# Kernel tuning notes

Hardware: AMD Instinct MI355X
Metric: run time of the kernel (lower is better)

Reference implementation:

```python
import jax, jax.numpy as jnp
import numpy as np

A = 8        # n_agents
NACT = 16    # n_actions
R = 64       # rnn_hidden_dim
OBS = 128    # obs_shape
ATTN = 64    # attn_dim
HID = 256    # hidden_dim
INP = 152    # input_shape = obs + n_actions + n_agents
E = 2048     # episode_num
TW = 1.0     # teammate_loss_weight
WW = 1.0     # world_loss_weight


def _lin(key, out_d, in_d):
    k1, k2 = jax.random.split(key)
    s = 1.0 / np.sqrt(in_d)
    w = jax.random.uniform(k1, (out_d, in_d), minval=-s, maxval=s, dtype=jnp.float32)
    b = jax.random.uniform(k2, (out_d,), minval=-s, maxval=s, dtype=jnp.float32)
    return w, b


def setup_inputs() -> dict:
    key = jax.random.key(0)
    ks = jax.random.split(key, 16)
    rows = E * A
    d = {}
    d['inputs'] = jax.random.normal(ks[0], (rows, INP), dtype=jnp.float32)
    d['hidden_state'] = jax.random.normal(ks[1], (rows, R), dtype=jnp.float32)
    d['obs'] = jax.random.normal(ks[2], (rows, OBS), dtype=jnp.float32)
    d['obs_next'] = jax.random.normal(ks[3], (rows, OBS), dtype=jnp.float32)
    d['u'] = jax.random.randint(ks[4], (rows, 1), 0, NACT, dtype=jnp.int64 if jax.config.jax_enable_x64 else jnp.int32)
    d['fc1_w'], d['fc1_b'] = _lin(ks[5], R, INP)
    d['gru_w_ih'], d['gru_b_ih'] = _lin(ks[6], 3 * R, R)
    d['gru_w_hh'], d['gru_b_hh'] = _lin(ks[7], 3 * R, R)
    d['tm_w1'], d['tm_b1'] = _lin(ks[8], HID, R + A)
    d['tm_w2'], d['tm_b2'] = _lin(ks[9], NACT, HID)
    d['wm_w1'], d['wm_b1'] = _lin(ks[10], HID, OBS + A * NACT)
    d['wm_w2'], d['wm_b2'] = _lin(ks[11], OBS, HID)
    d['wq_w'], d['wq_b'] = _lin(ks[12], ATTN, 2 * OBS)
    d['wk_w'], d['wk_b'] = _lin(ks[13], ATTN, NACT)
    d['wv1_w'], d['wv1_b'] = _lin(ks[14], ATTN, R + NACT)
    d['wv2_w'], d['wv2_b'] = _lin(ks[15], NACT, ATTN)
    return d


def reference(inputs, hidden_state, obs, obs_next, u,
              fc1_w, fc1_b, gru_w_ih, gru_b_ih, gru_w_hh, gru_b_hh,
              tm_w1, tm_b1, tm_w2, tm_b2,
              wm_w1, wm_b1, wm_w2, wm_b2,
              wq_w, wq_b, wk_w, wk_b, wv1_w, wv1_b, wv2_w, wv2_b):
    sg = jax.lax.stop_gradient
    rows = inputs.shape[0]
    Ep = rows // A  # episode_num

    # --- GRU agent trunk ---
    x = jax.nn.relu(inputs @ fc1_w.T + fc1_b)
    h_in = hidden_state.reshape(-1, R)
    gi = x @ gru_w_ih.T + gru_b_ih
    gh = h_in @ gru_w_hh.T + gru_b_hh
    i_r, i_z, i_n = jnp.split(gi, 3, axis=-1)
    h_r, h_z, h_n = jnp.split(gh, 3, axis=-1)
    r = jax.nn.sigmoid(i_r + h_r)
    z = jax.nn.sigmoid(i_z + h_z)
    n = jnp.tanh(i_n + r * h_n)
    h = (1.0 - z) * n + z * h_in  # (rows, R)

    eyeA = jnp.eye(A, dtype=h.dtype)
    off = 1.0 - eyeA  # (A,A) zero on diagonal

    # --- teammate model: h_repeat[e,i,j] = h[e,j] with diagonal zeroed ---
    hd = sg(h).reshape(Ep, A, R)
    hr = jnp.broadcast_to(hd[:, None, :, :], (Ep, A, A, R)) * off[None, :, :, None]
    dj = jnp.broadcast_to(eyeA[None, None], (Ep, A, A, A)) * off[None, :, :, None]
    inp_t = jnp.concatenate([hr.reshape(-1, R), dj.reshape(-1, A)], axis=-1)
    actions = jax.nn.relu(inp_t @ tm_w1.T + tm_b1) @ tm_w2.T + tm_b2  # (Ep*A*A, NACT)

    # --- teammate CE loss (masked mean over all Ep*A*A rows) ---
    labels = jnp.broadcast_to(u.reshape(Ep, 1, A), (Ep, A, A)).reshape(-1)
    mask = jnp.broadcast_to(off[None], (Ep, A, A)).reshape(-1)
    logp = jax.nn.log_softmax(actions, axis=-1)
    ce = -jnp.take_along_axis(logp, labels[:, None], axis=1)[:, 0]
    loss1 = (ce * mask).mean() * TW

    # --- mask own action, world model ---
    am = (actions.reshape(Ep, A, A, NACT) * off[None, :, :, None]).reshape(rows, A, NACT)
    am_det = sg(am)
    w_in = jnp.concatenate([obs, am_det.reshape(rows, A * NACT)], axis=-1)
    o_next_hat = jax.nn.relu(w_in @ wm_w1.T + wm_b1) @ wm_w2.T + wm_b2  # (rows, OBS)
    loss2 = jnp.mean((o_next_hat - obs_next) ** 2) * WW

    # --- reflection: masked attention aggregation over teammates ---
    query = jnp.concatenate([obs, sg(o_next_hat)], axis=-1) @ wq_w.T + wq_b  # (rows, ATTN)
    key = (am_det.reshape(-1, NACT) @ wk_w.T + wk_b).reshape(rows, A, ATTN)
    hrep = jnp.broadcast_to(h.reshape(Ep, 1, A, R), (Ep, A, A, R)).reshape(-1, R)
    inps_v = jnp.concatenate([hrep, am_det.reshape(-1, NACT)], axis=-1)
    value = (jax.nn.relu(inps_v @ wv1_w.T + wv1_b) @ wv2_w.T + wv2_b).reshape(rows, A, NACT)
    scores = jnp.einsum('bd,bjd->bj', query / jnp.sqrt(jnp.float32(ATTN)), key).reshape(Ep, A, A)
    scores = jnp.where(eyeA[None].astype(bool), jnp.float32(-1e9), scores)  # self-exclusion
    attn = jax.nn.softmax(scores, axis=-1).reshape(rows, A, 1)
    q_reflect = jnp.sum(value * attn, axis=1)  # (rows, NACT)

    return q_reflect, h, loss1, loss2
```

## Files before the change

kernel.cpp:

```cpp
#include <hip/hip_runtime.h>
#include <math.h>

#define E_NUM 2048
#define A_N   8
#define ROWS  (E_NUM*A_N)
#define TRUNK_BLOCKS 512
#define TRUNK_EXTRA  108

typedef __attribute__((ext_vector_type(8))) short bf16x8;
typedef __attribute__((ext_vector_type(4))) float f32x4;

__device__ __forceinline__ unsigned short f2bf(float x) {
  unsigned int u = __float_as_uint(x);
  return (unsigned short)((u + 0x7FFFu + ((u >> 16) & 1u)) >> 16);
}
__device__ __forceinline__ ushort4 f2bf4(float4 v) {
  return make_ushort4(f2bf(v.x), f2bf(v.y), f2bf(v.z), f2bf(v.w));
}
__device__ __forceinline__ float bf2f(unsigned short u) {
  return __uint_as_float(((unsigned int)u) << 16);
}
#define MFMA16(a,b,c) __builtin_amdgcn_mfma_f32_16x16x32_bf16(a,b,c,0,0,0)

#define T_WK   0
#define T_WV1  1024
#define T_WV2  6144
#define TMB    7168
#define B_WM1  9216
#define B_WM2  41984
#define B_WQ   58368
#define B_TM1  66560
#define B_TM2  74752
#define B_FC1  76800
#define B_WIH  81920
#define B_WHH  88064
#define O_ACT  94208
#define O_QRY  356352
#define O_L1P  1404928
#define O_L2P  1405440

#define DO_H   262144
#define DO_L1  1310720
#define DO_L2  1310721

#define LD4(p) (*(const float4*)(p))

struct PrepP {
  const float* tsrc[3]; int tO[3], tK[3], tOff[3];
  const float* ssrc[8]; int sO[8], sK[8], sKs[8], sSt[8], sOff[8];
  const float* tm_w1; const float* tm_b1;
};

__global__ __launch_bounds__(256) void k_prep(PrepP p, float* __restrict__ ws,
                                              unsigned short* __restrict__ wsu) {
  int bid = blockIdx.x;
  int m = 5 + (bid >> 4), sub = bid & 15;
  const float* src = p.ssrc[m];
  unsigned short* dst = wsu + p.sOff[m];
  int K = p.sK[m], Ks = p.sKs[m], stride = p.sSt[m], n = p.sO[m] * K, S = K >> 5;
  for (int f = sub * 256 + threadIdx.x; f < n; f += 16 * 256) {
    int j = f & 7, l = (f >> 3) & 63, rest = f >> 9;
    int s = rest % S, c = rest / S;
    int row = c * 16 + (l & 15), col = s * 32 + ((l >> 4) << 3) + j;
    dst[f] = (col < Ks) ? f2bf(src[row * stride + col]) : (unsigned short)0;
  }
}

__global__ __launch_bounds__(512, 4) void k_trunk(
    const float* __restrict__ inp, const float* __restrict__ hin,
    const unsigned short* __restrict__ fc1bf, const unsigned short* __restrict__ wihbf,
    const unsigned short* __restrict__ whhbf,
    const float* __restrict__ fc1_b, const float* __restrict__ bih, const float* __restrict__ bhh,
    float* __restrict__ hout, PrepP p, float* __restrict__ ws_f,
    unsigned short* __restrict__ wsu)
{
  __shared__ __align__(16) unsigned short in_b[32 * 168];
  __shared__ __align__(16) unsigned short x_b[32 * 72];
  __shared__ __align__(16) unsigned short h_b[32 * 72];
  int tid = threadIdx.x, w = tid >> 6, lane = tid & 63;
  int lo = lane & 15, hi = lane >> 4;

  if (blockIdx.x >= TRUNK_BLOCKS) {
    int eb = blockIdx.x - TRUNK_BLOCKS;
    if (eb < 24) {
      int b = eb >> 3, sl = eb & 7;
      const float* s = p.tsrc[b];
      float* d = ws_f + p.tOff[b];
      int O = p.tO[b], K = p.tK[b], n = O * K;
      for (int i = sl * 512 + tid; i < n; i += 8 * 512) {
        int o = i / K, k = i - o * K;
        d[k * O + o] = s[i];
      }
    } else if (eb < 104) {
      int q = eb - 24, m = q >> 4, sub = q & 15;
      const float* src = p.ssrc[m];
      unsigned short* dst = wsu + p.sOff[m];
      int K = p.sK[m], Ks = p.sKs[m], stride = p.sSt[m], n = p.sO[m] * K, S = K >> 5;
      for (int f = sub * 512 + tid; f < n; f += 16 * 512) {
        int j = f & 7, l = (f >> 3) & 63, rest = f >> 9;
        int s = rest % S, c = rest / S;
        int row = c * 16 + (l & 15), col = s * 32 + ((l >> 4) << 3) + j;
        dst[f] = (col < Ks) ? f2bf(src[row * stride + col]) : (unsigned short)0;
      }
    } else {
      int i = (eb - 104) * 512 + tid;
      int j = i >> 8, o = i & 255;
      ws_f[TMB + i] = p.tm_b1[o] + p.tm_w1[o * 72 + 64 + j];
    }
    return;
  }

  int row0 = blockIdx.x * 32;
  int c = w & 3, rt = w >> 2;

  for (int i = tid; i < 1216; i += 512) {
    int e = i << 2;
    int r = e / 152, cc = e - r * 152;
    float4 v = LD4(inp + (size_t)(row0 + r) * 152 + cc);
    *(ushort4*)(in_b + r * 168 + cc) = f2bf4(v);
  }
  if (tid < 256) { int r = tid >> 3, cc = tid & 7; in_b[r * 168 + 152 + cc] = 0; }
  {
    int r = tid >> 4, cc = (tid & 15) << 2;
    float4 v = LD4(hin + (size_t)(row0 + r) * 64 + cc);
    *(ushort4*)(h_b + r * 72 + cc) = f2bf4(v);
  }
  __syncthreads();

  bf16x8 wf1[5];
#pragma unroll
  for (int s = 0; s < 5; s++)
    wf1[s] = *(const bf16x8*)(fc1bf + (size_t)((c * 5 + s) * 64 + lane) * 8);
  f32x4 acc = {0, 0, 0, 0};
#pragma unroll
  for (int s = 0; s < 5; s++) {
    bf16x8 af = *(const bf16x8*)(in_b + (rt * 16 + lo) * 168 + s * 32 + hi * 8);
    acc = MFMA16(af, wf1[s], acc);
  }
  float fb = fc1_b[16 * c + lo];
#pragma unroll
  for (int r = 0; r < 4; r++)
    x_b[(rt * 16 + hi * 4 + r) * 72 + 16 * c + lo] = f2bf(fmaxf(acc[r] + fb, 0.f));
  __syncthreads();

  bf16x8 wfi[3][2], wfh[3][2];
#pragma unroll
  for (int t = 0; t < 3; t++)
#pragma unroll
    for (int s = 0; s < 2; s++) {
      int chunk = c + 4 * t;
      wfi[t][s] = *(const bf16x8*)(wihbf + (size_t)((chunk * 2 + s) * 64 + lane) * 8);
      wfh[t][s] = *(const bf16x8*)(whhbf + (size_t)((chunk * 2 + s) * 64 + lane) * 8);
    }
  f32x4 ai[3], ah[3];
#pragma unroll
  for (int t = 0; t < 3; t++) { ai[t] = {0,0,0,0}; ah[t] = {0,0,0,0}; }
#pragma unroll
  for (int s = 0; s < 2; s++) {
    bf16x8 ax  = *(const bf16x8*)(x_b + (rt * 16 + lo) * 72 + s * 32 + hi * 8);
    bf16x8 ahv = *(const bf16x8*)(h_b + (rt * 16 + lo) * 72 + s * 32 + hi * 8);
#pragma unroll
    for (int t = 0; t < 3; t++) {
      ai[t] = MFMA16(ax,  wfi[t][s], ai[t]);
      ah[t] = MFMA16(ahv, wfh[t][s], ah[t]);
    }
  }
  int col = 16 * c + lo;
  float b_ir = bih[col],       b_hr = bhh[col];
  float b_iz = bih[64 + col],  b_hz = bhh[64 + col];
  float b_in = bih[128 + col], b_hn = bhh[128 + col];
#pragma unroll
  for (int r = 0; r < 4; r++) {
    size_t grow = (size_t)(row0 + rt * 16 + hi * 4 + r);
    float rg = 1.f / (1.f + expf(-(ai[0][r] + b_ir + ah[0][r] + b_hr)));
    float zg = 1.f / (1.f + expf(-(ai[1][r] + b_iz + ah[1][r] + b_hz)));
    float ng = tanhf(fmaf(rg, ah[2][r] + b_hn, ai[2][r] + b_in));
    float h0 = hin[grow * 64 + col];
    hout[grow * 64 + col] = (1.f - zg) * ng + zg * h0;
  }
}

__global__ __launch_bounds__(512, 4) void k_tm(
    const float* __restrict__ h,
    const unsigned short* __restrict__ w1b, const unsigned short* __restrict__ w2b,
    const float* __restrict__ tmB, const float* __restrict__ b2,
    const int* __restrict__ u,
    float* __restrict__ act, float* __restrict__ l1p)
{
  __shared__ __align__(16) unsigned short in_s[32 * 72];
  __shared__ __align__(16) unsigned short hid_s[32 * 264];
  __shared__ float red[512];
  int tid = threadIdx.x, w = tid >> 6, lane = tid & 63;
  int lo = lane & 15, hi = lane >> 4;
  int row0 = blockIdx.x * 32;
  {
    int r = tid >> 4, cc = (tid & 15) << 2;
    float4 v = LD4(h + (size_t)(row0 + r) * 64 + cc);
    *(ushort4*)(in_s + r * 72 + cc) = f2bf4(v);
  }
  bf16x8 wf1[2][2];
#pragma unroll
  for (int cc = 0; cc < 2; cc++)
#pragma unroll
    for (int s = 0; s < 2; s++)
      wf1[cc][s] = *(const bf16x8*)(w1b + (size_t)(((2 * w + cc) * 2 + s) * 64 + lane) * 8);
  __syncthreads();
  f32x4 acc[2][2];
#pragma unroll
  for (int rt = 0; rt < 2; rt++) { acc[rt][0] = {0,0,0,0}; acc[rt][1] = {0,0,0,0}; }
#pragma unroll
  for (int s = 0; s < 2; s++)
#pragma unroll
    for (int rt = 0; rt < 2; rt++) {
      bf16x8 af = *(const bf16x8*)(in_s + (rt * 16 + lo) * 72 + s * 32 + hi * 8);
      acc[rt][0] = MFMA16(af, wf1[0][s], acc[rt][0]);
      acc[rt][1] = MFMA16(af, wf1[1][s], acc[rt][1]);
    }
#pragma unroll
  for (int rt = 0; rt < 2; rt++)
#pragma unroll
    for (int r = 0; r < 4; r++) {
      int rowl = rt * 16 + hi * 4 + r, j = (hi * 4 + r) & 7;
      float v0 = acc[rt][0][r] + tmB[j * 256 + 32 * w + lo];
      float v1 = acc[rt][1][r] + tmB[j * 256 + 32 * w + 16 + lo];
      hid_s[rowl * 264 + 32 * w + lo]      = f2bf(fmaxf(v0, 0.f));
      hid_s[rowl * 264 + 32 * w + 16 + lo] = f2bf(fmaxf(v1, 0.f));
    }
  __syncthreads();
  float ces = 0.f;
  if (w < 2) {
    bf16x8 wf2[8];
#pragma unroll
    for (int s = 0; s < 8; s++)
      wf2[s] = *(const bf16x8*)(w2b + (size_t)(s * 64 + lane) * 8);
    f32x4 a2 = {0, 0, 0, 0};
#pragma unroll
    for (int s = 0; s < 8; s++) {
      bf16x8 af = *(const bf16x8*)(hid_s + (w * 16 + lo) * 264 + s * 32 + hi * 8);
      a2 = MFMA16(af, wf2[s], a2);
    }
    float b2c = b2[lo];
#pragma unroll
    for (int r = 0; r < 4; r++) {
      int rowl = w * 16 + hi * 4 + r;
      float v = a2[r] + b2c;
      act[(size_t)(row0 + rowl) * 16 + lo] = v;
      float m = v;
      m = fmaxf(m, __shfl_xor(m, 1));
      m = fmaxf(m, __shfl_xor(m, 2));
      m = fmaxf(m, __shfl_xor(m, 4));
      m = fmaxf(m, __shfl_xor(m, 8));
      float se = expf(v - m);
      se += __shfl_xor(se, 1);
      se += __shfl_xor(se, 2);
      se += __shfl_xor(se, 4);
      se += __shfl_xor(se, 8);
      int lbl = u[row0 + rowl];
      float vl = __shfl(v, (lane & 48) + lbl);
      if (lo == 0) ces += -(vl - m - logf(se));
    }
  }
  red[tid] = ces;
  __syncthreads();
  for (int st = 256; st > 0; st >>= 1) {
    if (tid < st) red[tid] += red[tid + st];
    __syncthreads();
  }
  if (tid == 0) l1p[blockIdx.x] = red[0];
}

__global__ __launch_bounds__(512, 4) void k_wm(
    const float* __restrict__ obs, const float* __restrict__ act,
    const unsigned short* __restrict__ w1b, const unsigned short* __restrict__ w2b,
    const unsigned short* __restrict__ wqb,
    const float* __restrict__ b1, const float* __restrict__ b2, const float* __restrict__ bq,
    const float* __restrict__ obsn,
    unsigned short* __restrict__ qryb, float* __restrict__ l2p)
{
  __shared__ __align__(16) unsigned short in_s[32 * 264];
  __shared__ __align__(16) unsigned short q_in[32 * 264];
  __shared__ __align__(16) unsigned short act_bs[4 * 128];
  __shared__ float red[512];
  int tid = threadIdx.x, w = tid >> 6, lane = tid & 63;
  int lo = lane & 15, hi = lane >> 4;
  int row0 = blockIdx.x * 32, e0 = row0 >> 3;
  if (tid < 128) {
    float4 v = LD4(act + (size_t)e0 * 128 + (tid << 2));
    *(ushort4*)(act_bs + (tid << 2)) = f2bf4(v);
  }
  for (int i = tid; i < 1024; i += 512) {
    int r = i >> 5, c = (i & 31) << 2;
    float4 v = LD4(obs + (size_t)(row0 + r) * 128 + c);
    ushort4 u4 = f2bf4(v);
    *(ushort4*)(in_s + r * 264 + c) = u4;
    *(ushort4*)(q_in + r * 264 + c) = u4;
  }
  bf16x8 wf1[2][8], wf2[8];
#pragma unroll
  for (int cc = 0; cc < 2; cc++)
#pragma unroll
    for (int s = 0; s < 8; s++)
      wf1[cc][s] = *(const bf16x8*)(w1b + (size_t)(((2 * w + cc) * 8 + s) * 64 + lane) * 8);
#pragma unroll
  for (int s = 0; s < 8; s++)
    wf2[s] = *(const bf16x8*)(w2b + (size_t)((w * 8 + s) * 64 + lane) * 8);
  __syncthreads();
  for (int i = tid; i < 1024; i += 512) {
    int r = i >> 5, c = (i & 31) << 2;
    int j = c >> 4, ii = r & 7;
    ushort4 v = (j == ii) ? make_ushort4(0, 0, 0, 0)
                          : *(const ushort4*)(act_bs + (r >> 3) * 128 + c);
    *(ushort4*)(in_s + r * 264 + 128 + c) = v;
  }
  __syncthreads();
  f32x4 acc[2][2];
#pragma unroll
  for (int rt = 0; rt < 2; rt++) { acc[rt][0] = {0,0,0,0}; acc[rt][1] = {0,0,0,0}; }
#pragma unroll
  for (int s = 0; s < 8; s++)
#pragma unroll
    for (int rt = 0; rt < 2; rt++) {
      bf16x8 af = *(const bf16x8*)(in_s + (rt * 16 + lo) * 264 + s * 32 + hi * 8);
      acc[rt][0] = MFMA16(af, wf1[0][s], acc[rt][0]);
      acc[rt][1] = MFMA16(af, wf1[1][s], acc[rt][1]);
    }
  float b1a = b1[32 * w + lo], b1b = b1[32 * w + 16 + lo];
  __syncthreads();
#pragma unroll
  for (int rt = 0; rt < 2; rt++)
#pragma unroll
    for (int r = 0; r < 4; r++) {
      int rowl = rt * 16 + hi * 4 + r;
      in_s[rowl * 264 + 32 * w + lo]      = f2bf(fmaxf(acc[rt][0][r] + b1a, 0.f));
      in_s[rowl * 264 + 32 * w + 16 + lo] = f2bf(fmaxf(acc[rt][1][r] + b1b, 0.f));
    }
  __syncthreads();
  f32x4 acc2[2];
  acc2[0] = {0, 0, 0, 0}; acc2[1] = {0, 0, 0, 0};
#pragma unroll
  for (int s = 0; s < 8; s++)
#pragma unroll
    for (int rt = 0; rt < 2; rt++) {
      bf16x8 af = *(const bf16x8*)(in_s + (rt * 16 + lo) * 264 + s * 32 + hi * 8);
      acc2[rt] = MFMA16(af, wf2[s], acc2[rt]);
    }
  int col = 16 * w + lo;
  float b2c = b2[col];
  float ms = 0.f;
#pragma unroll
  for (int rt = 0; rt < 2; rt++)
#pragma unroll
    for (int r = 0; r < 4; r++) {
      int rowl = rt * 16 + hi * 4 + r;
      float v = acc2[rt][r] + b2c;
      q_in[rowl * 264 + 128 + col] = f2bf(v);
      float d = v - obsn[(size_t)(row0 + rowl) * 128 + col];
      ms = fmaf(d, d, ms);
    }
  __syncthreads();
  {
    int c = w & 3, rt = w >> 2;
    bf16x8 wf3[8];
#pragma unroll
    for (int s = 0; s < 8; s++)
      wf3[s] = *(const bf16x8*)(wqb + (size_t)((c * 8 + s) * 64 + lane) * 8);
    f32x4 aq = {0, 0, 0, 0};
#pragma unroll
    for (int s = 0; s < 8; s++) {
      bf16x8 af = *(const bf16x8*)(q_in + (rt * 16 + lo) * 264 + s * 32 + hi * 8);
      aq = MFMA16(af, wf3[s], aq);
    }
    float bqc = bq[16 * c + lo];
#pragma unroll
    for (int r = 0; r < 4; r++) {
      int row = row0 + rt * 16 + hi * 4 + r;
      qryb[(size_t)row * 64 + 16 * c + lo] = f2bf(aq[r] + bqc);
    }
  }
  red[tid] = ms;
  __syncthreads();
  for (int st = 256; st > 0; st >>= 1) {
    if (tid < st) red[tid] += red[tid + st];
    __syncthreads();
  }
  if (tid == 0) l2p[blockIdx.x] = red[0];
}

__global__ __launch_bounds__(512, 4) void k_kva(
    const float* __restrict__ h, const float* __restrict__ act,
    const float* __restrict__ ws, const float* __restrict__ bk,
    const float* __restrict__ bv1, const float* __restrict__ bv2,
    const unsigned short* __restrict__ qryb, const float* __restrict__ l1p,
    const float* __restrict__ l2p, float* __restrict__ qout)
{
  __shared__ __align__(16) float in_s[32 * 80];
  __shared__ __align__(16) float hid_s[32 * 64];
  __shared__ __align__(16) float key_s[32 * 68];
  __shared__ float val_s[32 * 16];
  __shared__ float qs[8][64];
  __shared__ float red2[512];
  int tid = threadIdx.x, w = tid >> 6, lane = tid & 63;
  int row0 = blockIdx.x * 32;
  if (blockIdx.x == 0) {
    red2[tid] = l1p[tid];
    __syncthreads();
    for (int s = 256; s > 0; s >>= 1) {
      if (tid < s) red2[tid] += red2[tid + s];
      __syncthreads();
    }
    float S1 = red2[0];
    __syncthreads();
    red2[tid] = l2p[tid];
    __syncthreads();
    for (int s = 256; s > 0; s >>= 1) {
      if (tid < s) red2[tid] += red2[tid + s];
      __syncthreads();
    }
    if (tid == 0) {
      qout[DO_L1] = S1 * 7.f / 131072.f;
      qout[DO_L2] = red2[0] / 2097152.f;
    }
    __syncthreads();
  }
  {
    int r = tid >> 4, c = (tid & 15) << 2;
    *(float4*)(in_s + r * 80 + c) = LD4(h + (size_t)(row0 + r) * 64 + c);
  }
  if (tid < 128) {
    int r = tid >> 2, c = (tid & 3) << 2;
    *(float4*)(in_s + r * 80 + 64 + c) = LD4(act + (size_t)(row0 + r) * 16 + c);
  }
  float qreg[4];
#pragma unroll
  for (int rr = 0; rr < 4; rr++)
    qreg[rr] = bf2f(qryb[(size_t)(row0 + w * 4 + rr) * 64 + lane]);
  __syncthreads();
  const float* w1T = ws + T_WV1;
  const float* w2T = ws + T_WV2;
  const float* wkT = ws + T_WK;
  float acc[4], ka[4];
#pragma unroll
  for (int r = 0; r < 4; r++) { acc[r] = bv1[lane]; ka[r] = bk[lane]; }
  for (int k = 0; k < 80; k += 4) {
    float b[4];
#pragma unroll
    for (int j = 0; j < 4; j++) b[j] = w1T[(k + j) * 64 + lane];
#pragma unroll
    for (int r = 0; r < 4; r++) {
      float4 a = LD4(in_s + (w * 4 + r) * 80 + k);
      acc[r] = fmaf(a.x, b[0], fmaf(a.y, b[1], fmaf(a.z, b[2], fmaf(a.w, b[3], acc[r]))));
    }
  }
  for (int k = 0; k < 16; k += 4) {
    float b[4];
#pragma unroll
    for (int j = 0; j < 4; j++) b[j] = wkT[(k + j) * 64 + lane];
#pragma unroll
    for (int r = 0; r < 4; r++) {
      float4 a = LD4(in_s + (w * 4 + r) * 80 + 64 + k);
      ka[r] = fmaf(a.x, b[0], fmaf(a.y, b[1], fmaf(a.z, b[2], fmaf(a.w, b[3], ka[r]))));
    }
  }
#pragma unroll
  for (int r = 0; r < 4; r++) {
    hid_s[(w * 4 + r) * 64 + lane] = fmaxf(acc[r], 0.f);
    key_s[(w * 4 + r) * 68 + lane] = ka[r];
  }
  {
    int col = lane & 15, kq = lane >> 4;
    float a2[4] = {0, 0, 0, 0};
    for (int kk = 0; kk < 16; kk += 4) {
      int k = kq * 16 + kk;
      float b[4];
#pragma unroll
      for (int j = 0; j < 4; j++) b[j] = w2T[(k + j) * 16 + col];
#pragma unroll
      for (int r = 0; r < 4; r++) {
        float4 a = LD4(hid_s + (w * 4 + r) * 64 + k);
        a2[r] = fmaf(a.x, b[0], fmaf(a.y, b[1], fmaf(a.z, b[2], fmaf(a.w, b[3], a2[r]))));
      }
    }
#pragma unroll
    for (int r = 0; r < 4; r++) {
      a2[r] += __shfl_xor(a2[r], 16);
      a2[r] += __shfl_xor(a2[r], 32);
    }
    if (lane < 16)
#pragma unroll
      for (int r = 0; r < 4; r++) val_s[(w * 4 + r) * 16 + col] = a2[r] + bv2[col];
  }
  __syncthreads();
  {
    int ep = w >> 1;
    int j = lane >> 3, p = lane & 7;
    for (int q2 = 0; q2 < 4; q2++) {
      int bl = w * 4 + q2;
      int rr = bl & 7;
      qs[w][lane] = qreg[q2];
      const float* krow = key_s + (ep * 8 + j) * 68;
      float s = 0.f;
#pragma unroll
      for (int t = 0; t < 8; t++) {
        int d = p * 8 + t;
        s = fmaf(qs[w][d], krow[d], s);
      }
      s += __shfl_xor(s, 1);
      s += __shfl_xor(s, 2);
      s += __shfl_xor(s, 4);
      float score = (j == rr) ? -1e9f : s * 0.125f;
      float sc[8];
      float m = -1e30f;
#pragma unroll
      for (int jj = 0; jj < 8; jj++) {
        sc[jj] = __shfl(score, jj * 8);
        m = fmaxf(m, sc[jj]);
      }
      float ssum = 0.f;
#pragma unroll
      for (int jj = 0; jj < 8; jj++) { sc[jj] = expf(sc[jj] - m); ssum += sc[jj]; }
      float inv = 1.f / ssum;
      int c = lane & 15, g = lane >> 4;
      const float* vb = val_s + ep * 128;
      float outv = sc[g] * inv * vb[g * 16 + c] + sc[g + 4] * inv * vb[(g + 4) * 16 + c];
      outv += __shfl_xor(outv, 16);
      outv += __shfl_xor(outv, 32);
      if (lane < 16) qout[(size_t)(row0 + bl) * 16 + lane] = outv;
    }
  }
}

extern "C" void kernel_launch(void* const* d_in, const int* in_sizes, int n_in,
                              void* d_out, int out_size, void* d_ws, size_t ws_size,
                              hipStream_t stream) {
  const float* inputs   = (const float*)d_in[0];
  const float* hidden   = (const float*)d_in[1];
  const float* obs      = (const float*)d_in[2];
  const float* obs_next = (const float*)d_in[3];
  const int*   u        = (const int*)d_in[4];
  const float* fc1_w = (const float*)d_in[5];   const float* fc1_b = (const float*)d_in[6];
  const float* wih   = (const float*)d_in[7];   const float* bih   = (const float*)d_in[8];
  const float* whh   = (const float*)d_in[9];   const float* bhh   = (const float*)d_in[10];
  const float* tm_w1 = (const float*)d_in[11];  const float* tm_b1 = (const float*)d_in[12];
  const float* tm_w2 = (const float*)d_in[13];  const float* tm_b2 = (const float*)d_in[14];
  const float* wm_w1 = (const float*)d_in[15];  const float* wm_b1 = (const float*)d_in[16];
  const float* wm_w2 = (const float*)d_in[17];  const float* wm_b2 = (const float*)d_in[18];
  const float* wq_w  = (const float*)d_in[19];  const float* wq_b  = (const float*)d_in[20];
  const float* wk_w  = (const float*)d_in[21];  const float* wk_b  = (const float*)d_in[22];
  const float* wv1_w = (const float*)d_in[23];  const float* wv1_b = (const float*)d_in[24];
  const float* wv2_w = (const float*)d_in[25];  const float* wv2_b = (const float*)d_in[26];

  float* ws   = (float*)d_ws;
  unsigned short* wsu = (unsigned short*)d_ws;
  float* out  = (float*)d_out;
  float* hbuf = out + DO_H;

  PrepP p;
  const float* tsr[3] = {wk_w, wv1_w, wv2_w};
  int tO[3]  = {64, 64, 16};
  int tK[3]  = {16, 80, 64};
  int tOf[3] = {T_WK, T_WV1, T_WV2};
  for (int i = 0; i < 3; i++) { p.tsrc[i] = tsr[i]; p.tO[i] = tO[i]; p.tK[i] = tK[i]; p.tOff[i] = tOf[i]; }
  const float* ssr[8] = {wm_w1, wm_w2, wq_w, tm_w1, tm_w2, fc1_w, wih, whh};
  int sO[8]  = {256, 128, 64, 256, 16, 64, 192, 192};
  int sK[8]  = {256, 256, 256, 64, 256, 160, 64, 64};
  int sKs[8] = {256, 256, 256, 64, 256, 152, 64, 64};
  int sSt[8] = {256, 256, 256, 72, 256, 152, 64, 64};
  int sOf[8] = {B_WM1*2, B_WM2*2, B_WQ*2, B_TM1*2, B_TM2*2, B_FC1*2, B_WIH*2, B_WHH*2};
  for (int i = 0; i < 8; i++) {
    p.ssrc[i] = ssr[i]; p.sO[i] = sO[i]; p.sK[i] = sK[i];
    p.sKs[i] = sKs[i]; p.sSt[i] = sSt[i]; p.sOff[i] = sOf[i];
  }
  p.tm_w1 = tm_w1; p.tm_b1 = tm_b1;

  k_prep<<<48, 256, 0, stream>>>(p, ws, wsu);
  k_trunk<<<TRUNK_BLOCKS + TRUNK_EXTRA, 512, 0, stream>>>(inputs, hidden,
      wsu + B_FC1*2, wsu + B_WIH*2, wsu + B_WHH*2, fc1_b, bih, bhh, hbuf, p, ws, wsu);
  k_tm<<<ROWS / 32, 512, 0, stream>>>(hbuf, wsu + B_TM1*2, wsu + B_TM2*2,
      ws + TMB, tm_b2, u, ws + O_ACT, ws + O_L1P);
  k_wm<<<ROWS / 32, 512, 0, stream>>>(obs, ws + O_ACT,
      wsu + B_WM1*2, wsu + B_WM2*2, wsu + B_WQ*2, wm_b1, wm_b2, wq_b, obs_next,
      wsu + O_QRY * 2, ws + O_L2P);
  k_kva<<<ROWS / 32, 512, 0, stream>>>(hbuf, ws + O_ACT, ws, wk_b, wv1_b, wv2_b,
      wsu + O_QRY * 2, ws + O_L1P, ws + O_L2P, out);
}
```

Measured before the change: 45.67 us.

## Drop weight-prep kernel and convert fp32 weights to bf16 fragments in-kernel

Removes the k_prep launch and the extra prep blocks inside k_trunk that repacked and transposed weights into bf16 MFMA-fragment layout in workspace. Each compute kernel now loads fp32 weights directly from their original row-major layout and converts them to bf16 fragments in registers. The tm bias+one-hot table is recomputed per thread from tm_w1 columns. This saves a kernel launch and a serialized prep pass, at the cost of redundant per-block conversion work and twice the bytes per weight load, with less coalesced access.

```diff
diff --git a/kernel.cpp b/kernel.cpp
--- a/kernel.cpp
+++ b/kernel.cpp
@@ -4,8 +4,6 @@
 #define E_NUM 2048
 #define A_N   8
 #define ROWS  (E_NUM*A_N)
-#define TRUNK_BLOCKS 512
-#define TRUNK_EXTRA  108
 
 typedef __attribute__((ext_vector_type(8))) short bf16x8;
 typedef __attribute__((ext_vector_type(4))) float f32x4;
@@ -21,95 +19,38 @@
   return __uint_as_float(((unsigned int)u) << 16);
 }
 #define MFMA16(a,b,c) __builtin_amdgcn_mfma_f32_16x16x32_bf16(a,b,c,0,0,0)
-
-#define T_WK   0
-#define T_WV1  1024
-#define T_WV2  6144
-#define TMB    7168
-#define B_WM1  9216
-#define B_WM2  41984
-#define B_WQ   58368
-#define B_TM1  66560
-#define B_TM2  74752
-#define B_FC1  76800
-#define B_WIH  81920
-#define B_WHH  88064
-#define O_ACT  94208
-#define O_QRY  356352
-#define O_L1P  1404928
-#define O_L2P  1405440
+#define LD4(p) (*(const float4*)(p))
+
+__device__ __forceinline__ bf16x8 ldfrag(const float* __restrict__ W, int stride, int row, int col) {
+  const float* pp = W + row * stride + col;
+  float4 a = LD4(pp), b = LD4(pp + 4);
+  bf16x8 r;
+  r[0] = (short)f2bf(a.x); r[1] = (short)f2bf(a.y); r[2] = (short)f2bf(a.z); r[3] = (short)f2bf(a.w);
+  r[4] = (short)f2bf(b.x); r[5] = (short)f2bf(b.y); r[6] = (short)f2bf(b.z); r[7] = (short)f2bf(b.w);
+  return r;
+}
+
+#define O_ACT  0
+#define O_QRY  262144
+#define O_L1P  786432
+#define O_L2P  786944
 
 #define DO_H   262144
 #define DO_L1  1310720
 #define DO_L2  1310721
 
-#define LD4(p) (*(const float4*)(p))
-
-struct PrepP {
-  const float* tsrc[3]; int tO[3], tK[3], tOff[3];
-  const float* ssrc[8]; int sO[8], sK[8], sKs[8], sSt[8], sOff[8];
-  const float* tm_w1; const float* tm_b1;
-};
-
-__global__ __launch_bounds__(256) void k_prep(PrepP p, float* __restrict__ ws,
-                                              unsigned short* __restrict__ wsu) {
-  int bid = blockIdx.x;
-  int m = 5 + (bid >> 4), sub = bid & 15;
-  const float* src = p.ssrc[m];
-  unsigned short* dst = wsu + p.sOff[m];
-  int K = p.sK[m], Ks = p.sKs[m], stride = p.sSt[m], n = p.sO[m] * K, S = K >> 5;
-  for (int f = sub * 256 + threadIdx.x; f < n; f += 16 * 256) {
-    int j = f & 7, l = (f >> 3) & 63, rest = f >> 9;
-    int s = rest % S, c = rest / S;
-    int row = c * 16 + (l & 15), col = s * 32 + ((l >> 4) << 3) + j;
-    dst[f] = (col < Ks) ? f2bf(src[row * stride + col]) : (unsigned short)0;
-  }
-}
-
 __global__ __launch_bounds__(512, 4) void k_trunk(
     const float* __restrict__ inp, const float* __restrict__ hin,
-    const unsigned short* __restrict__ fc1bf, const unsigned short* __restrict__ wihbf,
-    const unsigned short* __restrict__ whhbf,
+    const float* __restrict__ fc1_w, const float* __restrict__ wih,
+    const float* __restrict__ whh,
     const float* __restrict__ fc1_b, const float* __restrict__ bih, const float* __restrict__ bhh,
-    float* __restrict__ hout, PrepP p, float* __restrict__ ws_f,
-    unsigned short* __restrict__ wsu)
+    float* __restrict__ hout)
 {
   __shared__ __align__(16) unsigned short in_b[32 * 168];
   __shared__ __align__(16) unsigned short x_b[32 * 72];
   __shared__ __align__(16) unsigned short h_b[32 * 72];
   int tid = threadIdx.x, w = tid >> 6, lane = tid & 63;
   int lo = lane & 15, hi = lane >> 4;
-
-  if (blockIdx.x >= TRUNK_BLOCKS) {
-    int eb = blockIdx.x - TRUNK_BLOCKS;
-    if (eb < 24) {
-      int b = eb >> 3, sl = eb & 7;
-      const float* s = p.tsrc[b];
-      float* d = ws_f + p.tOff[b];
-      int O = p.tO[b], K = p.tK[b], n = O * K;
-      for (int i = sl * 512 + tid; i < n; i += 8 * 512) {
-        int o = i / K, k = i - o * K;
-        d[k * O + o] = s[i];
-      }
-    } else if (eb < 104) {
-      int q = eb - 24, m = q >> 4, sub = q & 15;
-      const float* src = p.ssrc[m];
-      unsigned short* dst = wsu + p.sOff[m];
-      int K = p.sK[m], Ks = p.sKs[m], stride = p.sSt[m], n = p.sO[m] * K, S = K >> 5;
-      for (int f = sub * 512 + tid; f < n; f += 16 * 512) {
-        int j = f & 7, l = (f >> 3) & 63, rest = f >> 9;
-        int s = rest % S, c = rest / S;
-        int row = c * 16 + (l & 15), col = s * 32 + ((l >> 4) << 3) + j;
-        dst[f] = (col < Ks) ? f2bf(src[row * stride + col]) : (unsigned short)0;
-      }
-    } else {
-      int i = (eb - 104) * 512 + tid;
-      int j = i >> 8, o = i & 255;
-      ws_f[TMB + i] = p.tm_b1[o] + p.tm_w1[o * 72 + 64 + j];
-    }
-    return;
-  }
-
   int row0 = blockIdx.x * 32;
   int c = w & 3, rt = w >> 2;
 
@@ -129,8 +70,14 @@
 
   bf16x8 wf1[5];
 #pragma unroll
-  for (int s = 0; s < 5; s++)
-    wf1[s] = *(const bf16x8*)(fc1bf + (size_t)((c * 5 + s) * 64 + lane) * 8);
+  for (int s = 0; s < 5; s++) {
+    if (s == 4 && hi == 3) {
+      bf16x8 z = {0, 0, 0, 0, 0, 0, 0, 0};
+      wf1[s] = z;
+    } else {
+      wf1[s] = ldfrag(fc1_w, 152, c * 16 + lo, s * 32 + hi * 8);
+    }
+  }
   f32x4 acc = {0, 0, 0, 0};
 #pragma unroll
   for (int s = 0; s < 5; s++) {
@@ -149,8 +96,8 @@
 #pragma unroll
     for (int s = 0; s < 2; s++) {
       int chunk = c + 4 * t;
-      wfi[t][s] = *(const bf16x8*)(wihbf + (size_t)((chunk * 2 + s) * 64 + lane) * 8);
-      wfh[t][s] = *(const bf16x8*)(whhbf + (size_t)((chunk * 2 + s) * 64 + lane) * 8);
+      wfi[t][s] = ldfrag(wih, 64, chunk * 16 + lo, s * 32 + hi * 8);
+      wfh[t][s] = ldfrag(whh, 64, chunk * 16 + lo, s * 32 + hi * 8);
     }
   f32x4 ai[3], ah[3];
 #pragma unroll
@@ -182,8 +129,8 @@
 
 __global__ __launch_bounds__(512, 4) void k_tm(
     const float* __restrict__ h,
-    const unsigned short* __restrict__ w1b, const unsigned short* __restrict__ w2b,
-    const float* __restrict__ tmB, const float* __restrict__ b2,
+    const float* __restrict__ tm_w1, const float* __restrict__ tm_w2,
+    const float* __restrict__ tm_b1, const float* __restrict__ b2,
     const int* __restrict__ u,
     float* __restrict__ act, float* __restrict__ l1p)
 {
@@ -203,7 +150,18 @@
   for (int cc = 0; cc < 2; cc++)
 #pragma unroll
     for (int s = 0; s < 2; s++)
-      wf1[cc][s] = *(const bf16x8*)(w1b + (size_t)(((2 * w + cc) * 2 + s) * 64 + lane) * 8);
+      wf1[cc][s] = ldfrag(tm_w1, 72, (2 * w + cc) * 16 + lo, s * 32 + hi * 8);
+  int col0 = 32 * w + lo, col1 = 32 * w + 16 + lo;
+  float oh0[8], oh1[8];
+  {
+    float4 a = LD4(tm_w1 + col0 * 72 + 64), b = LD4(tm_w1 + col0 * 72 + 68);
+    oh0[0] = a.x; oh0[1] = a.y; oh0[2] = a.z; oh0[3] = a.w;
+    oh0[4] = b.x; oh0[5] = b.y; oh0[6] = b.z; oh0[7] = b.w;
+    float4 c2 = LD4(tm_w1 + col1 * 72 + 64), d = LD4(tm_w1 + col1 * 72 + 68);
+    oh1[0] = c2.x; oh1[1] = c2.y; oh1[2] = c2.z; oh1[3] = c2.w;
+    oh1[4] = d.x; oh1[5] = d.y; oh1[6] = d.z; oh1[7] = d.w;
+  }
+  float b1c0 = tm_b1[col0], b1c1 = tm_b1[col1];
   __syncthreads();
   f32x4 acc[2][2];
 #pragma unroll
@@ -221,10 +179,10 @@
 #pragma unroll
     for (int r = 0; r < 4; r++) {
       int rowl = rt * 16 + hi * 4 + r, j = (hi * 4 + r) & 7;
-      float v0 = acc[rt][0][r] + tmB[j * 256 + 32 * w + lo];
-      float v1 = acc[rt][1][r] + tmB[j * 256 + 32 * w + 16 + lo];
-      hid_s[rowl * 264 + 32 * w + lo]      = f2bf(fmaxf(v0, 0.f));
-      hid_s[rowl * 264 + 32 * w + 16 + lo] = f2bf(fmaxf(v1, 0.f));
+      float v0 = acc[rt][0][r] + b1c0 + oh0[j];
+      float v1 = acc[rt][1][r] + b1c1 + oh1[j];
+      hid_s[rowl * 264 + col0] = f2bf(fmaxf(v0, 0.f));
+      hid_s[rowl * 264 + col1] = f2bf(fmaxf(v1, 0.f));
     }
   __syncthreads();
   float ces = 0.f;
@@ -232,7 +190,7 @@
     bf16x8 wf2[8];
 #pragma unroll
     for (int s = 0; s < 8; s++)
-      wf2[s] = *(const bf16x8*)(w2b + (size_t)(s * 64 + lane) * 8);
+      wf2[s] = ldfrag(tm_w2, 256, lo, s * 32 + hi * 8);
     f32x4 a2 = {0, 0, 0, 0};
 #pragma unroll
     for (int s = 0; s < 8; s++) {
@@ -271,8 +229,8 @@
 
 __global__ __launch_bounds__(512, 4) void k_wm(
     const float* __restrict__ obs, const float* __restrict__ act,
-    const unsigned short* __restrict__ w1b, const unsigned short* __restrict__ w2b,
-    const unsigned short* __restrict__ wqb,
+    const float* __restrict__ wm_w1, const float* __restrict__ wm_w2,
+    const float* __restrict__ wq_w,
     const float* __restrict__ b1, const float* __restrict__ b2, const float* __restrict__ bq,
     const float* __restrict__ obsn,
     unsigned short* __restrict__ qryb, float* __restrict__ l2p)
@@ -300,10 +258,10 @@
   for (int cc = 0; cc < 2; cc++)
 #pragma unroll
     for (int s = 0; s < 8; s++)
-      wf1[cc][s] = *(const bf16x8*)(w1b + (size_t)(((2 * w + cc) * 8 + s) * 64 + lane) * 8);
+      wf1[cc][s] = ldfrag(wm_w1, 256, (2 * w + cc) * 16 + lo, s * 32 + hi * 8);
 #pragma unroll
   for (int s = 0; s < 8; s++)
-    wf2[s] = *(const bf16x8*)(w2b + (size_t)((w * 8 + s) * 64 + lane) * 8);
+    wf2[s] = ldfrag(wm_w2, 256, w * 16 + lo, s * 32 + hi * 8);
   __syncthreads();
   for (int i = tid; i < 1024; i += 512) {
     int r = i >> 5, c = (i & 31) << 2;
@@ -363,7 +321,7 @@
     bf16x8 wf3[8];
 #pragma unroll
     for (int s = 0; s < 8; s++)
-      wf3[s] = *(const bf16x8*)(wqb + (size_t)((c * 8 + s) * 64 + lane) * 8);
+      wf3[s] = ldfrag(wq_w, 256, c * 16 + lo, s * 32 + hi * 8);
     f32x4 aq = {0, 0, 0, 0};
 #pragma unroll
     for (int s = 0; s < 8; s++) {
@@ -388,7 +346,8 @@
 
 __global__ __launch_bounds__(512, 4) void k_kva(
     const float* __restrict__ h, const float* __restrict__ act,
-    const float* __restrict__ ws, const float* __restrict__ bk,
+    const float* __restrict__ wk_w, const float* __restrict__ wv1_w,
+    const float* __restrict__ wv2_w, const float* __restrict__ bk,
     const float* __restrict__ bv1, const float* __restrict__ bv2,
     const unsigned short* __restrict__ qryb, const float* __restrict__ l1p,
     const float* __restrict__ l2p, float* __restrict__ qout)
@@ -435,16 +394,12 @@
   for (int rr = 0; rr < 4; rr++)
     qreg[rr] = bf2f(qryb[(size_t)(row0 + w * 4 + rr) * 64 + lane]);
   __syncthreads();
-  const float* w1T = ws + T_WV1;
-  const float* w2T = ws + T_WV2;
-  const float* wkT = ws + T_WK;
   float acc[4], ka[4];
 #pragma unroll
   for (int r = 0; r < 4; r++) { acc[r] = bv1[lane]; ka[r] = bk[lane]; }
   for (int k = 0; k < 80; k += 4) {
-    float b[4];
-#pragma unroll
-    for (int j = 0; j < 4; j++) b[j] = w1T[(k + j) * 64 + lane];
+    float4 bw = LD4(wv1_w + lane * 80 + k);
+    float b[4] = {bw.x, bw.y, bw.z, bw.w};
 #pragma unroll
     for (int r = 0; r < 4; r++) {
       float4 a = LD4(in_s + (w * 4 + r) * 80 + k);
@@ -452,9 +407,8 @@
     }
   }
   for (int k = 0; k < 16; k += 4) {
-    float b[4];
-#pragma unroll
-    for (int j = 0; j < 4; j++) b[j] = wkT[(k + j) * 64 + lane];
+    float4 bw = LD4(wk_w + lane * 16 + k);
+    float b[4] = {bw.x, bw.y, bw.z, bw.w};
 #pragma unroll
     for (int r = 0; r < 4; r++) {
       float4 a = LD4(in_s + (w * 4 + r) * 80 + 64 + k);
@@ -471,9 +425,8 @@
     float a2[4] = {0, 0, 0, 0};
     for (int kk = 0; kk < 16; kk += 4) {
       int k = kq * 16 + kk;
-      float b[4];
-#pragma unroll
-      for (int j = 0; j < 4; j++) b[j] = w2T[(k + j) * 16 + col];
+      float4 bw = LD4(wv2_w + col * 64 + k);
+      float b[4] = {bw.x, bw.y, bw.z, bw.w};
 #pragma unroll
       for (int r = 0; r < 4; r++) {
         float4 a = LD4(hid_s + (w * 4 + r) * 64 + k);
@@ -554,32 +507,12 @@
   float* out  = (float*)d_out;
   float* hbuf = out + DO_H;
 
-  PrepP p;
-  const float* tsr[3] = {wk_w, wv1_w, wv2_w};
-  int tO[3]  = {64, 64, 16};
-  int tK[3]  = {16, 80, 64};
-  int tOf[3] = {T_WK, T_WV1, T_WV2};
-  for (int i = 0; i < 3; i++) { p.tsrc[i] = tsr[i]; p.tO[i] = tO[i]; p.tK[i] = tK[i]; p.tOff[i] = tOf[i]; }
-  const float* ssr[8] = {wm_w1, wm_w2, wq_w, tm_w1, tm_w2, fc1_w, wih, whh};
-  int sO[8]  = {256, 128, 64, 256, 16, 64, 192, 192};
-  int sK[8]  = {256, 256, 256, 64, 256, 160, 64, 64};
-  int sKs[8] = {256, 256, 256, 64, 256, 152, 64, 64};
-  int sSt[8] = {256, 256, 256, 72, 256, 152, 64, 64};
-  int sOf[8] = {B_WM1*2, B_WM2*2, B_WQ*2, B_TM1*2, B_TM2*2, B_FC1*2, B_WIH*2, B_WHH*2};
-  for (int i = 0; i < 8; i++) {
-    p.ssrc[i] = ssr[i]; p.sO[i] = sO[i]; p.sK[i] = sK[i];
-    p.sKs[i] = sKs[i]; p.sSt[i] = sSt[i]; p.sOff[i] = sOf[i];
-  }
-  p.tm_w1 = tm_w1; p.tm_b1 = tm_b1;
-
-  k_prep<<<48, 256, 0, stream>>>(p, ws, wsu);
-  k_trunk<<<TRUNK_BLOCKS + TRUNK_EXTRA, 512, 0, stream>>>(inputs, hidden,
-      wsu + B_FC1*2, wsu + B_WIH*2, wsu + B_WHH*2, fc1_b, bih, bhh, hbuf, p, ws, wsu);
-  k_tm<<<ROWS / 32, 512, 0, stream>>>(hbuf, wsu + B_TM1*2, wsu + B_TM2*2,
-      ws + TMB, tm_b2, u, ws + O_ACT, ws + O_L1P);
-  k_wm<<<ROWS / 32, 512, 0, stream>>>(obs, ws + O_ACT,
-      wsu + B_WM1*2, wsu + B_WM2*2, wsu + B_WQ*2, wm_b1, wm_b2, wq_b, obs_next,
-      wsu + O_QRY * 2, ws + O_L2P);
-  k_kva<<<ROWS / 32, 512, 0, stream>>>(hbuf, ws + O_ACT, ws, wk_b, wv1_b, wv2_b,
-      wsu + O_QRY * 2, ws + O_L1P, ws + O_L2P, out);
-}
+  k_trunk<<<ROWS / 32, 512, 0, stream>>>(inputs, hidden, fc1_w, wih, whh,
+      fc1_b, bih, bhh, hbuf);
+  k_tm<<<ROWS / 32, 512, 0, stream>>>(hbuf, tm_w1, tm_w2, tm_b1, tm_b2, u,
+      ws + O_ACT, ws + O_L1P);
+  k_wm<<<ROWS / 32, 512, 0, stream>>>(obs, ws + O_ACT, wm_w1, wm_w2, wq_w,
+      wm_b1, wm_b2, wq_b, obs_next, wsu + O_QRY * 2, ws + O_L2P);
+  k_kva<<<ROWS / 32, 512, 0, stream>>>(hbuf, ws + O_ACT, wk_w, wv1_w, wv2_w,
+      wk_b, wv1_b, wv2_b, wsu + O_QRY * 2, ws + O_L1P, ws + O_L2P, out);
+}
```

Result: slower. 154.1 us (+237.5%).
